# Optimization experiments

Hardware: AMD Instinct MI355X
Metric: run time of the kernel (lower is better)

The kernel has to match this reference:

```python
import jax, jax.numpy as jnp
import numpy as np

E = 8            # n_experts
TEMP = float(np.e)
N_ACTIVE = 5     # max(1, int(8 * 0.7))
EPS = 1e-8


def setup_inputs() -> dict:
    key = jax.random.key(0)
    ks = jax.random.split(key, 6)
    N, D, H, O = 8192, 1024, 2048, 1024

    def init(k, shape, fan_in):
        return (jax.random.normal(k, shape, jnp.float32) / np.sqrt(fan_in)).astype(jnp.float32)

    return {
        "x": jax.random.normal(ks[0], (N, D), jnp.float32),
        "gate_W": init(ks[1], (D, E), D),
        "gate_b": jnp.zeros((E,), jnp.float32),
        "W1": init(ks[2], (E, D, H), D),
        "b1": jnp.zeros((E, H), jnp.float32),
        "W2": init(ks[3], (E, H, H), H),
        "b2": jnp.zeros((E, H), jnp.float32),
        "W3": init(ks[4], (E, H, O), H),
        "b3": jnp.zeros((E, O), jnp.float32),
    }


def reference(x, gate_W, gate_b, W1, b1, W2, b2, W3, b3):
    # Boltzmann gate: softmax(scores / T), keep top n_active, renormalize.
    scores = (x @ gate_W + gate_b) / TEMP            # [N, E]
    probs = jax.nn.softmax(scores, axis=-1)          # [N, E]
    _, idx = jax.lax.top_k(probs, N_ACTIVE)          # [N, n_active]
    rows = jnp.arange(probs.shape[0])[:, None]
    mask = jnp.zeros_like(probs).at[rows, idx].set(1.0)
    w = probs * mask
    w = w / (w.sum(axis=-1, keepdims=True) + EPS)    # [N, E]

    # Dense all-expert MLP (dropout is identity in eval mode).
    h = jax.nn.relu(jnp.einsum('nd,edh->enh', x, W1) + b1[:, None, :])   # [E, N, H]
    h = jax.nn.relu(jnp.einsum('enh,ehk->enk', h, W2) + b2[:, None, :])  # [E, N, H]
    out = jnp.einsum('enh,eho->eno', h, W3) + b3[:, None, :]             # [E, N, O]

    # Weighted combine over experts.
    return jnp.einsum('ne,eno->no', w, out)          # [N, O]
```

## Files before the change

### kernel.cpp

```cpp
#include <hip/hip_runtime.h>

#define N_ROWS 8192
#define DIM_D  1024
#define DIM_H  2048
#define DIM_O  1024
#define NEXP   8
#define NACT   5
#define MAX_TILES 168

typedef _Float16 f16x8 __attribute__((ext_vector_type(8)));
typedef float    f32x4 __attribute__((ext_vector_type(4)));

__device__ __forceinline__ void gload_lds16(const void* g, void* l) {
  __builtin_amdgcn_global_load_lds(
      (const __attribute__((address_space(1))) void*)g,
      (__attribute__((address_space(3))) void*)l, 16, 0, 0);
}

__global__ void convert_x_kernel(const float* __restrict__ in,
                                 _Float16* __restrict__ out, int n) {
  int i = (blockIdx.x * 256 + threadIdx.x) * 8;
  if (i >= n) return;
  const float4 a = *(const float4*)(in + i);
  const float4 b = *(const float4*)(in + i + 4);
  f16x8 v;
  v[0] = (_Float16)a.x; v[1] = (_Float16)a.y; v[2] = (_Float16)a.z; v[3] = (_Float16)a.w;
  v[4] = (_Float16)b.x; v[5] = (_Float16)b.y; v[6] = (_Float16)b.z; v[7] = (_Float16)b.w;
  *(f16x8*)(out + i) = v;
}

__global__ void zero_f32_kernel(float* __restrict__ p, int n4) {
  int i = blockIdx.x * 256 + threadIdx.x;
  if (i < n4) ((float4*)p)[i] = make_float4(0.f, 0.f, 0.f, 0.f);
}
__global__ void zero_counts_kernel(int* __restrict__ cnt) {
  if (threadIdx.x < NEXP) cnt[threadIdx.x] = 0;
}

__global__ void transpose_to_f16(const float* __restrict__ in,
                                 _Float16* __restrict__ out, int R, int C) {
  in  += (size_t)blockIdx.z * R * C;
  out += (size_t)blockIdx.z * R * C;
  __shared__ float tile[32][33];
  const int tx = threadIdx.x & 31, ty = threadIdx.x >> 5;
  const int c0 = blockIdx.x * 32, r0 = blockIdx.y * 32;
#pragma unroll
  for (int j = 0; j < 32; j += 8)
    tile[ty + j][tx] = in[(size_t)(r0 + ty + j) * C + c0 + tx];
  __syncthreads();
#pragma unroll
  for (int j = 0; j < 32; j += 8)
    out[(size_t)(c0 + ty + j) * R + r0 + tx] = (_Float16)tile[tx][ty + j];
}

__global__ void gate_kernel(const float* __restrict__ x, const float* __restrict__ gW,
                            const float* __restrict__ gb, float* __restrict__ wout) {
  const int lane = threadIdx.x & 63;
  const int row  = blockIdx.x * 4 + (threadIdx.x >> 6);
  float acc[8] = {0.f,0.f,0.f,0.f,0.f,0.f,0.f,0.f};
  const float* xr = x + (size_t)row * DIM_D;
  for (int d = lane; d < DIM_D; d += 64) {
    float xv = xr[d];
    const float4* g4 = (const float4*)(gW + d * 8);
    float4 a = g4[0], b = g4[1];
    acc[0] += xv * a.x; acc[1] += xv * a.y; acc[2] += xv * a.z; acc[3] += xv * a.w;
    acc[4] += xv * b.x; acc[5] += xv * b.y; acc[6] += xv * b.z; acc[7] += xv * b.w;
  }
#pragma unroll
  for (int off = 32; off > 0; off >>= 1) {
#pragma unroll
    for (int e = 0; e < 8; ++e) acc[e] += __shfl_xor(acc[e], off);
  }
  const float invT = 0.36787944117144233f;
  float s[8], mx = -1e30f;
#pragma unroll
  for (int e = 0; e < 8; ++e) { s[e] = (acc[e] + gb[e]) * invT; mx = fmaxf(mx, s[e]); }
  float p[8], sum = 0.f;
#pragma unroll
  for (int e = 0; e < 8; ++e) { p[e] = expf(s[e] - mx); sum += p[e]; }
  float inv = 1.f / sum;
#pragma unroll
  for (int e = 0; e < 8; ++e) p[e] *= inv;
  unsigned keep = 0;
  for (int it = 0; it < NACT; ++it) {
    int best = 0; float bv = -1.f;
#pragma unroll
    for (int e = 0; e < 8; ++e)
      if (!(keep & (1u << e)) && p[e] > bv) { bv = p[e]; best = e; }
    keep |= 1u << best;
  }
  float ks = 0.f;
#pragma unroll
  for (int e = 0; e < 8; ++e) if (keep & (1u << e)) ks += p[e];
  const float winv = 1.f / (ks + 1e-8f);
  if (lane < 8)
    wout[(size_t)row * 8 + lane] = (keep & (1u << lane)) ? p[lane] * winv : 0.f;
}

__global__ void count_kernel(const float* __restrict__ wg, int* __restrict__ cnt) {
  const int row = blockIdx.x * 256 + threadIdx.x;
  const int lane = threadIdx.x & 63;
#pragma unroll
  for (int e = 0; e < NEXP; ++e) {
    const bool keep = wg[(size_t)row * 8 + e] > 0.f;
    unsigned long long m = __ballot(keep);
    if (lane == 0 && m) atomicAdd(&cnt[e], __popcll(m));
  }
}

__global__ void offsets_kernel(const int* __restrict__ cnt, int* __restrict__ cursor,
                               int* __restrict__ offs, int* __restrict__ ntiles,
                               int2* __restrict__ ttab, int* __restrict__ rlist) {
  __shared__ int soffs[NEXP], scnt[NEXP];
  if (threadIdx.x == 0) {
    int off = 0, k = 0;
    for (int e = 0; e < NEXP; ++e) {
      offs[e] = off; soffs[e] = off; scnt[e] = cnt[e];
      cursor[e] = 0;
      const int nt = (cnt[e] + 255) >> 8;
      for (int t2 = 0; t2 < nt; ++t2) { ttab[k] = make_int2(e, off + t2 * 256); ++k; }
      off += nt << 8;
    }
    *ntiles = k;
  }
  __syncthreads();
#pragma unroll
  for (int e = 0; e < NEXP; ++e) {
    const int lo = soffs[e] + scnt[e];
    const int hi = soffs[e] + ((scnt[e] + 255) & ~255);
    for (int i = lo + (int)threadIdx.x; i < hi; i += 256) rlist[i] = 0;
  }
}

__global__ void place_kernel(const float* __restrict__ wg, const int* __restrict__ offs,
                             int* __restrict__ cursor, int* __restrict__ rlist,
                             int* __restrict__ pos) {
  const int row = blockIdx.x * 256 + threadIdx.x;
  const int lane = threadIdx.x & 63;
#pragma unroll
  for (int e = 0; e < NEXP; ++e) {
    const bool keep = wg[(size_t)row * 8 + e] > 0.f;
    unsigned long long m = __ballot(keep);
    if (m) {
      const int leader = __ffsll(m) - 1;
      const int pre = __popcll(m & ((1ull << lane) - 1ull));
      int base = 0;
      if (lane == leader) base = atomicAdd(&cursor[e], __popcll(m));
      base = __shfl(base, leader);
      if (keep) {
        const int idx = offs[e] + base + pre;
        rlist[idx] = row;
        pos[(size_t)row * 8 + e] = idx;
      }
    }
  }
}

__global__ void combine_kernel(const float* __restrict__ wg, const int* __restrict__ pos,
                               const _Float16* __restrict__ y, float* __restrict__ out) {
  const int tid = blockIdx.x * 256 + threadIdx.x;
  const int row = tid >> 7, c8 = (tid & 127) * 8;
  float a[8] = {0.f,0.f,0.f,0.f,0.f,0.f,0.f,0.f};
#pragma unroll
  for (int e = 0; e < NEXP; ++e) {
    const float w = wg[(size_t)row * 8 + e];
    if (w > 0.f) {
      const int p = pos[(size_t)row * 8 + e];
      const f16x8 v = *(const f16x8*)(y + (size_t)p * DIM_O + c8);
#pragma unroll
      for (int j = 0; j < 8; ++j) a[j] += w * (float)v[j];
    }
  }
  float4* o4 = (float4*)(out + (size_t)row * DIM_O + c8);
  o4[0] = make_float4(a[0], a[1], a[2], a[3]);
  o4[1] = make_float4(a[4], a[5], a[6], a[7]);
}

#define MFMA16 __builtin_amdgcn_mfma_f32_16x16x32_f16
template <int MODE>
__global__ __launch_bounds__(512, 2) void gemm8(
    const _Float16* __restrict__ A, const _Float16* __restrict__ BtAll,
    _Float16* __restrict__ C, const float* __restrict__ biasAll,
    const int* __restrict__ rlist, const int2* __restrict__ ttab,
    const int* __restrict__ ntilesp, int N, int K) {
  const int ti = blockIdx.y;
  if (ti >= *ntilesp) return;
  const int2 tt = ttab[ti];
  const int e = tt.x, grow0 = tt.y;
  const int col0 = blockIdx.x * 256;

  __shared__ _Float16 sA[2][256 * 64];
  __shared__ _Float16 sB[2][256 * 64];

  const int t = threadIdx.x, wid = t >> 6, lane = t & 63;
  const int wm = wid >> 2, wn = wid & 3;
  const int l15 = lane & 15, lg = lane >> 4;

  const _Float16* Bt = BtAll + (size_t)e * N * K;

  const int srow = wid * 8 + (lane >> 3);
  const int scol = ((lane & 7) ^ (lane >> 3)) << 3;
  size_t arow[4], brow[4];
#pragma unroll
  for (int c = 0; c < 4; ++c) {
    const int r = c * 64 + srow;
    const int gr = (MODE == 0) ? rlist[grow0 + r] : (grow0 + r);
    arow[c] = (size_t)gr * K;
    brow[c] = (size_t)(col0 + r) * K;
  }
  const int ldst = wid * 512;

  auto STAGE = [&](int buf, int kt) {
    const int kofs = kt * 64 + scol;
#pragma unroll
    for (int c = 0; c < 4; ++c)
      gload_lds16(A + arow[c] + kofs, &sA[buf][c * 4096 + ldst]);
#pragma unroll
    for (int c = 0; c < 4; ++c)
      gload_lds16(Bt + brow[c] + kofs, &sB[buf][c * 4096 + ldst]);
  };

  const int ck0 = ((lg * 16) ^ ((l15 & 7) << 4)) >> 1;
  const int ck1 = ((64 + lg * 16) ^ ((l15 & 7) << 4)) >> 1;

  f32x4 acc[8][4] = {};
  const int NT = K >> 6;
  STAGE(0, 0);
  STAGE(1, 1);

  for (int tk = 0; tk < NT; ++tk) {
    const int buf = tk & 1;
    if (tk + 1 < NT) asm volatile("s_waitcnt vmcnt(8)" ::: "memory");
    else             asm volatile("s_waitcnt vmcnt(0)" ::: "memory");
    __builtin_amdgcn_sched_barrier(0);
    __builtin_amdgcn_s_barrier();
    __builtin_amdgcn_sched_barrier(0);

    const _Float16* pA = &sA[buf][wm * 128 * 64];
    const _Float16* pB = &sB[buf][wn * 64 * 64];

    f16x8 af[4][2], bf0[2][2], bf1[2][2];
#pragma unroll
    for (int m = 0; m < 4; ++m) {
      af[m][0] = *(const f16x8*)(pA + (m * 16 + l15) * 64 + ck0);
      af[m][1] = *(const f16x8*)(pA + (m * 16 + l15) * 64 + ck1);
    }
#pragma unroll
    for (int n = 0; n < 2; ++n) {
      bf0[n][0] = *(const f16x8*)(pB + (n * 16 + l15) * 64 + ck0);
      bf0[n][1] = *(const f16x8*)(pB + (n * 16 + l15) * 64 + ck1);
    }
    __builtin_amdgcn_s_setprio(1);
#pragma unroll
    for (int m = 0; m < 4; ++m)
#pragma unroll
      for (int n = 0; n < 2; ++n) {
        acc[m][n] = MFMA16(af[m][0], bf0[n][0], acc[m][n], 0, 0, 0);
        acc[m][n] = MFMA16(af[m][1], bf0[n][1], acc[m][n], 0, 0, 0);
      }
    __builtin_amdgcn_s_setprio(0);
#pragma unroll
    for (int n = 0; n < 2; ++n) {
      bf1[n][0] = *(const f16x8*)(pB + ((n + 2) * 16 + l15) * 64 + ck0);
      bf1[n][1] = *(const f16x8*)(pB + ((n + 2) * 16 + l15) * 64 + ck1);
    }
    __builtin_amdgcn_s_setprio(1);
#pragma unroll
    for (int m = 0; m < 4; ++m)
#pragma unroll
      for (int n = 0; n < 2; ++n) {
        acc[m][n + 2] = MFMA16(af[m][0], bf1[n][0], acc[m][n + 2], 0, 0, 0);
        acc[m][n + 2] = MFMA16(af[m][1], bf1[n][1], acc[m][n + 2], 0, 0, 0);
      }
    __builtin_amdgcn_s_setprio(0);
#pragma unroll
    for (int m = 0; m < 4; ++m) {
      af[m][0] = *(const f16x8*)(pA + ((m + 4) * 16 + l15) * 64 + ck0);
      af[m][1] = *(const f16x8*)(pA + ((m + 4) * 16 + l15) * 64 + ck1);
    }
    __builtin_amdgcn_s_setprio(1);
#pragma unroll
    for (int m = 0; m < 4; ++m)
#pragma unroll
      for (int n = 0; n < 2; ++n) {
        acc[m + 4][n] = MFMA16(af[m][0], bf0[n][0], acc[m + 4][n], 0, 0, 0);
        acc[m + 4][n] = MFMA16(af[m][1], bf0[n][1], acc[m + 4][n], 0, 0, 0);
      }
#pragma unroll
    for (int m = 0; m < 4; ++m)
#pragma unroll
      for (int n = 0; n < 2; ++n) {
        acc[m + 4][n + 2] = MFMA16(af[m][0], bf1[n][0], acc[m + 4][n + 2], 0, 0, 0);
        acc[m + 4][n + 2] = MFMA16(af[m][1], bf1[n][1], acc[m + 4][n + 2], 0, 0, 0);
      }
    __builtin_amdgcn_s_setprio(0);

    __builtin_amdgcn_sched_barrier(0);
    __builtin_amdgcn_s_barrier();
    __builtin_amdgcn_sched_barrier(0);
    if (tk + 2 < NT) STAGE(buf, tk + 2);
  }

  const float* bias = biasAll + (size_t)e * N;
  float bv[4];
#pragma unroll
  for (int n = 0; n < 4; ++n) bv[n] = bias[col0 + wn * 64 + n * 16 + l15];
#pragma unroll
  for (int mi = 0; mi < 8; ++mi) {
#pragma unroll
    for (int n = 0; n < 4; ++n) {
      const int gc = col0 + wn * 64 + n * 16 + l15;
#pragma unroll
      for (int r = 0; r < 4; ++r) {
        const int grow = grow0 + wm * 128 + mi * 16 + lg * 4 + r;
        const float v = acc[mi][n][r] + bv[n];
        C[(size_t)grow * N + gc] = (_Float16)((MODE == 2) ? v : fmaxf(v, 0.f));
      }
    }
  }
}

__global__ void compact_old(const float* __restrict__ wg, int* __restrict__ cnt,
                            int* __restrict__ rowlist) {
  const int row = blockIdx.x * 256 + threadIdx.x;
  const int lane = threadIdx.x & 63;
#pragma unroll
  for (int e = 0; e < NEXP; ++e) {
    const float w = wg[(size_t)row * 8 + e];
    const bool keep = (w > 0.f);
    unsigned long long m = __ballot(keep);
    if (m) {
      const int leader = __ffsll(m) - 1;
      const int pre = __popcll(m & ((1ull << lane) - 1ull));
      int base = 0;
      if (lane == leader) base = atomicAdd(&cnt[e], __popcll(m));
      base = __shfl(base, leader);
      if (keep) rowlist[e * N_ROWS + base + pre] = row;
    }
  }
}

template <int MODE>
__global__ __launch_bounds__(256, 2) void gemm_nt(
    const _Float16* __restrict__ A, const _Float16* __restrict__ Bt,
    void* __restrict__ Cout, const float* __restrict__ bias,
    const float* __restrict__ wg, const int* __restrict__ rlist,
    const int* __restrict__ cntp, int e, int N, int K) {
  const int M = *cntp;
  const int row0 = blockIdx.y * 128, col0 = blockIdx.x * 128;
  if (row0 >= M) return;
  __shared__ _Float16 sA[128 * 64];
  __shared__ _Float16 sB[128 * 64];
  const int t = threadIdx.x;
  const int w = t >> 6, lane = t & 63;
  const int wm = w >> 1, wn = w & 1;
  const int l15 = lane & 15, lg = lane >> 4;
  size_t arow[4];
#pragma unroll
  for (int i = 0; i < 4; ++i) {
    const int chunk = i * 256 + t;
    int li = row0 + (chunk >> 3);
    if (li >= M && MODE == 0) li = M - 1;
    const int gr = (MODE == 0) ? rlist[li] : li;
    arow[i] = (size_t)gr * K;
  }
  f32x4 acc[4][4] = {};
  for (int kt = 0; kt < K; kt += 64) {
    __syncthreads();
#pragma unroll
    for (int i = 0; i < 4; ++i) {
      const int chunk = i * 256 + t;
      const int cb = (chunk & 7) * 8;
      gload_lds16(A + arow[i] + kt + cb, sA + (i * 256 + w * 64) * 8);
    }
#pragma unroll
    for (int i = 0; i < 4; ++i) {
      const int chunk = i * 256 + t;
      const int r = chunk >> 3, cb = (chunk & 7) * 8;
      gload_lds16(Bt + (size_t)(col0 + r) * K + kt + cb, sB + (i * 256 + w * 64) * 8);
    }
    __syncthreads();
#pragma unroll
    for (int k2 = 0; k2 < 2; ++k2) {
      f16x8 af[4], bf[4];
#pragma unroll
      for (int m = 0; m < 4; ++m)
        af[m] = *(const f16x8*)(sA + (wm * 64 + m * 16 + l15) * 64 + k2 * 32 + lg * 8);
#pragma unroll
      for (int n = 0; n < 4; ++n)
        bf[n] = *(const f16x8*)(sB + (wn * 64 + n * 16 + l15) * 64 + k2 * 32 + lg * 8);
#pragma unroll
      for (int m = 0; m < 4; ++m)
#pragma unroll
        for (int n = 0; n < 4; ++n)
          acc[m][n] = MFMA16(af[m], bf[n], acc[m][n], 0, 0, 0);
    }
  }
#pragma unroll
  for (int m = 0; m < 4; ++m) {
#pragma unroll
    for (int n = 0; n < 4; ++n) {
      const int gc = col0 + wn * 64 + n * 16 + l15;
      const float bvv = bias[gc];
#pragma unroll
      for (int r = 0; r < 4; ++r) {
        const int gr = row0 + wm * 64 + m * 16 + lg * 4 + r;
        float v = acc[m][n][r] + bvv;
        if (MODE == 3) {
          if (gr < M) {
            const int orow = rlist[gr];
            atomicAdd((float*)Cout + (size_t)orow * N + gc,
                      wg[(size_t)orow * 8 + e] * v);
          }
        } else {
          ((_Float16*)Cout)[(size_t)gr * N + gc] = (_Float16)fmaxf(v, 0.f);
        }
      }
    }
  }
}

extern "C" void kernel_launch(void* const* d_in, const int* in_sizes, int n_in,
                              void* d_out, int out_size, void* d_ws, size_t ws_size,
                              hipStream_t stream) {
  const float* x  = (const float*)d_in[0];
  const float* gW = (const float*)d_in[1];
  const float* gb = (const float*)d_in[2];
  const float* W1 = (const float*)d_in[3];
  const float* b1 = (const float*)d_in[4];
  const float* W2 = (const float*)d_in[5];
  const float* b2 = (const float*)d_in[6];
  const float* W3 = (const float*)d_in[7];
  const float* b3 = (const float*)d_in[8];
  float* out = (float*)d_out;

  char* ws = (char*)d_ws;
  const bool big = (ws_size >= 0x1E100000ULL);

  if (big) {
    float* wgate   = (float*)ws;
    int*   meta    = (int*)(ws + 0x40000);
    int*   cnt     = meta;
    int*   cursor  = meta + 8;
    int*   offs    = meta + 16;
    int*   ntiles  = meta + 24;
    int2*  ttab    = (int2*)(meta + 32);
    int*   pos     = (int*)(ws + 0x80000);
    int*   rlistg  = (int*)(ws + 0xC0000);
    _Float16* xh   = (_Float16*)(ws + 0x100000);
    _Float16* h1   = (_Float16*)(ws + 0x1100000);
    _Float16* h2   = (_Float16*)(ws + 0xB900000);
    _Float16* wt1  = (_Float16*)(ws + 0x16100000);
    _Float16* wt2  = (_Float16*)(ws + 0x18100000);
    _Float16* wt3  = (_Float16*)(ws + 0x1C100000);
    _Float16* y    = h1;

    convert_x_kernel<<<(N_ROWS * DIM_D) / (256 * 8), 256, 0, stream>>>(x, xh, N_ROWS * DIM_D);
    gate_kernel<<<N_ROWS / 4, 256, 0, stream>>>(x, gW, gb, wgate);
    zero_counts_kernel<<<1, 64, 0, stream>>>(cnt);
    count_kernel<<<N_ROWS / 256, 256, 0, stream>>>(wgate, cnt);
    offsets_kernel<<<1, 256, 0, stream>>>(cnt, cursor, offs, ntiles, ttab, rlistg);
    place_kernel<<<N_ROWS / 256, 256, 0, stream>>>(wgate, offs, cursor, rlistg, pos);

    transpose_to_f16<<<dim3(DIM_H / 32, DIM_D / 32, NEXP), 256, 0, stream>>>(W1, wt1, DIM_D, DIM_H);
    transpose_to_f16<<<dim3(DIM_H / 32, DIM_H / 32, NEXP), 256, 0, stream>>>(W2, wt2, DIM_H, DIM_H);
    transpose_to_f16<<<dim3(DIM_O / 32, DIM_H / 32, NEXP), 256, 0, stream>>>(W3, wt3, DIM_H, DIM_O);

    gemm8<0><<<dim3(DIM_H / 256, MAX_TILES), 512, 0, stream>>>(
        xh, wt1, h1, b1, rlistg, ttab, ntiles, DIM_H, DIM_D);
    gemm8<1><<<dim3(DIM_H / 256, MAX_TILES), 512, 0, stream>>>(
        h1, wt2, h2, b2, rlistg, ttab, ntiles, DIM_H, DIM_H);
    gemm8<2><<<dim3(DIM_O / 256, MAX_TILES), 512, 0, stream>>>(
        h2, wt3, y, b3, rlistg, ttab, ntiles, DIM_O, DIM_H);

    combine_kernel<<<(N_ROWS * 128) / 256, 256, 0, stream>>>(wgate, pos, y, out);
  } else {
    float*    wgate = (float*)ws;
    int*      cnt   = (int*)(ws + 0x40000);
    int*      rlist = (int*)(ws + 0x80000);
    _Float16* xh    = (_Float16*)(ws + 0x100000);
    _Float16* h1    = (_Float16*)(ws + 0x1100000);
    _Float16* h2    = (_Float16*)(ws + 0x3100000);
    _Float16* wt1   = (_Float16*)(ws + 0x5100000);
    _Float16* wt2   = (_Float16*)(ws + 0x5500000);
    _Float16* wt3   = (_Float16*)(ws + 0x5D00000);

    convert_x_kernel<<<(N_ROWS * DIM_D) / (256 * 8), 256, 0, stream>>>(x, xh, N_ROWS * DIM_D);
    gate_kernel<<<N_ROWS / 4, 256, 0, stream>>>(x, gW, gb, wgate);
    zero_counts_kernel<<<1, 64, 0, stream>>>(cnt);
    compact_old<<<N_ROWS / 256, 256, 0, stream>>>(wgate, cnt, rlist);
    zero_f32_kernel<<<(N_ROWS * DIM_O / 4 + 255) / 256, 256, 0, stream>>>(out, N_ROWS * DIM_O / 4);

    for (int e = 0; e < NEXP; ++e) {
      transpose_to_f16<<<dim3(DIM_H / 32, DIM_D / 32), 256, 0, stream>>>(
          W1 + (size_t)e * DIM_D * DIM_H, wt1, DIM_D, DIM_H);
      transpose_to_f16<<<dim3(DIM_H / 32, DIM_H / 32), 256, 0, stream>>>(
          W2 + (size_t)e * DIM_H * DIM_H, wt2, DIM_H, DIM_H);
      transpose_to_f16<<<dim3(DIM_O / 32, DIM_H / 32), 256, 0, stream>>>(
          W3 + (size_t)e * DIM_H * DIM_O, wt3, DIM_H, DIM_O);
      const int* ce = cnt + e;
      const int* re = rlist + e * N_ROWS;
      gemm_nt<0><<<dim3(DIM_H / 128, N_ROWS / 128), 256, 0, stream>>>(
          xh, wt1, h1, b1 + (size_t)e * DIM_H, wgate, re, ce, e, DIM_H, DIM_D);
      gemm_nt<1><<<dim3(DIM_H / 128, N_ROWS / 128), 256, 0, stream>>>(
          h1, wt2, h2, b2 + (size_t)e * DIM_H, wgate, re, ce, e, DIM_H, DIM_H);
      gemm_nt<3><<<dim3(DIM_O / 128, N_ROWS / 128), 256, 0, stream>>>(
          h2, wt3, out, b3 + (size_t)e * DIM_O, wgate, re, ce, e, DIM_O, DIM_H);
    }
  }
}
```

Baseline: 1.081 ms.

## Interleave staged global-to-LDS loads between MFMA quarters and remap tiles per XCD

The GEMM main loop now splits each prefetch of the next-but-one K tile into pieces (A rows 0/2, all of B, A rows 1/3). These are issued between the four MFMA quarters, separated by extra barriers, once the corresponding LDS region has been read. This replaces a single bulk stage at the end of each iteration and is meant to overlap memory traffic with compute. Block IDs are also remapped so that consecutive blocks scheduled round-robin on the 8 XCDs work on the same row tile, which is meant to improve L2 reuse. In exchange there are more barriers per iteration, and the kernel always issues dummy loads of tile 0 in the tail iterations.

```diff
diff --git a/kernel.cpp b/kernel.cpp
--- a/kernel.cpp
+++ b/kernel.cpp
@@ -183,11 +183,15 @@
     _Float16* __restrict__ C, const float* __restrict__ biasAll,
     const int* __restrict__ rlist, const int2* __restrict__ ttab,
     const int* __restrict__ ntilesp, int N, int K) {
-  const int ti = blockIdx.y;
+  const int ncol = gridDim.x;
+  const int b = blockIdx.y * ncol + blockIdx.x;
+  const int xcd = b & 7, idx = b >> 3;
+  const int ti = xcd * (MAX_TILES / 8) + idx / ncol;
+  const int colt = idx % ncol;
   if (ti >= *ntilesp) return;
   const int2 tt = ttab[ti];
   const int e = tt.x, grow0 = tt.y;
-  const int col0 = blockIdx.x * 256;
+  const int col0 = colt * 256;
 
   __shared__ _Float16 sA[2][256 * 64];
   __shared__ _Float16 sB[2][256 * 64];
@@ -210,14 +214,16 @@
   }
   const int ldst = wid * 512;
 
-  auto STAGE = [&](int buf, int kt) {
+  auto STAGE_A2 = [&](int sbuf, int kt, int c0_, int c1_) {
     const int kofs = kt * 64 + scol;
+    gload_lds16(A + arow[c0_] + kofs, &sA[sbuf][c0_ * 4096 + ldst]);
+    gload_lds16(A + arow[c1_] + kofs, &sA[sbuf][c1_ * 4096 + ldst]);
+  };
+  auto STAGE_B4 = [&](int sbuf, int kt) {
+    const int kofs = kt * 64 + scol;
 #pragma unroll
     for (int c = 0; c < 4; ++c)
-      gload_lds16(A + arow[c] + kofs, &sA[buf][c * 4096 + ldst]);
-#pragma unroll
-    for (int c = 0; c < 4; ++c)
-      gload_lds16(Bt + brow[c] + kofs, &sB[buf][c * 4096 + ldst]);
+      gload_lds16(Bt + brow[c] + kofs, &sB[sbuf][c * 4096 + ldst]);
   };
 
   const int ck0 = ((lg * 16) ^ ((l15 & 7) << 4)) >> 1;
@@ -225,81 +231,102 @@
 
   f32x4 acc[8][4] = {};
   const int NT = K >> 6;
-  STAGE(0, 0);
-  STAGE(1, 1);
+  const int k1 = (NT > 1) ? 1 : 0;
+
+  STAGE_A2(0, 0, 0, 1); STAGE_A2(0, 0, 2, 3); STAGE_B4(0, 0);
+  STAGE_A2(1, k1, 0, 2); STAGE_B4(1, k1); STAGE_A2(1, k1, 1, 3);
 
   for (int tk = 0; tk < NT; ++tk) {
     const int buf = tk & 1;
-    if (tk + 1 < NT) asm volatile("s_waitcnt vmcnt(8)" ::: "memory");
-    else             asm volatile("s_waitcnt vmcnt(0)" ::: "memory");
-    __builtin_amdgcn_sched_barrier(0);
-    __builtin_amdgcn_s_barrier();
-    __builtin_amdgcn_sched_barrier(0);
-
+    const int s2 = (tk + 2 < NT) ? tk + 2 : 0;
     const _Float16* pA = &sA[buf][wm * 128 * 64];
     const _Float16* pB = &sB[buf][wn * 64 * 64];
-
-    f16x8 af[4][2], bf0[2][2], bf1[2][2];
+    f16x8 a0[4][2], a1[4][2], b0[2][2], b1[2][2];
+
+    asm volatile("s_waitcnt vmcnt(8)" ::: "memory");
+    __builtin_amdgcn_sched_barrier(0);
+    __builtin_amdgcn_s_barrier();
+    __builtin_amdgcn_sched_barrier(0);
 #pragma unroll
     for (int m = 0; m < 4; ++m) {
-      af[m][0] = *(const f16x8*)(pA + (m * 16 + l15) * 64 + ck0);
-      af[m][1] = *(const f16x8*)(pA + (m * 16 + l15) * 64 + ck1);
+      a0[m][0] = *(const f16x8*)(pA + (m * 16 + l15) * 64 + ck0);
+      a0[m][1] = *(const f16x8*)(pA + (m * 16 + l15) * 64 + ck1);
     }
 #pragma unroll
     for (int n = 0; n < 2; ++n) {
-      bf0[n][0] = *(const f16x8*)(pB + (n * 16 + l15) * 64 + ck0);
-      bf0[n][1] = *(const f16x8*)(pB + (n * 16 + l15) * 64 + ck1);
-    }
+      b0[n][0] = *(const f16x8*)(pB + (n * 16 + l15) * 64 + ck0);
+      b0[n][1] = *(const f16x8*)(pB + (n * 16 + l15) * 64 + ck1);
+    }
+    asm volatile("s_waitcnt lgkmcnt(0)" ::: "memory");
+    __builtin_amdgcn_sched_barrier(0);
     __builtin_amdgcn_s_setprio(1);
 #pragma unroll
     for (int m = 0; m < 4; ++m)
 #pragma unroll
       for (int n = 0; n < 2; ++n) {
-        acc[m][n] = MFMA16(af[m][0], bf0[n][0], acc[m][n], 0, 0, 0);
-        acc[m][n] = MFMA16(af[m][1], bf0[n][1], acc[m][n], 0, 0, 0);
+        acc[m][n] = MFMA16(a0[m][0], b0[n][0], acc[m][n], 0, 0, 0);
+        acc[m][n] = MFMA16(a0[m][1], b0[n][1], acc[m][n], 0, 0, 0);
       }
     __builtin_amdgcn_s_setprio(0);
+
+    __builtin_amdgcn_sched_barrier(0);
+    __builtin_amdgcn_s_barrier();
+    __builtin_amdgcn_sched_barrier(0);
 #pragma unroll
     for (int n = 0; n < 2; ++n) {
-      bf1[n][0] = *(const f16x8*)(pB + ((n + 2) * 16 + l15) * 64 + ck0);
-      bf1[n][1] = *(const f16x8*)(pB + ((n + 2) * 16 + l15) * 64 + ck1);
-    }
+      b1[n][0] = *(const f16x8*)(pB + ((n + 2) * 16 + l15) * 64 + ck0);
+      b1[n][1] = *(const f16x8*)(pB + ((n + 2) * 16 + l15) * 64 + ck1);
+    }
+    STAGE_A2(buf, s2, 0, 2);
+    asm volatile("s_waitcnt lgkmcnt(0)" ::: "memory");
+    __builtin_amdgcn_sched_barrier(0);
     __builtin_amdgcn_s_setprio(1);
 #pragma unroll
     for (int m = 0; m < 4; ++m)
 #pragma unroll
       for (int n = 0; n < 2; ++n) {
-        acc[m][n + 2] = MFMA16(af[m][0], bf1[n][0], acc[m][n + 2], 0, 0, 0);
-        acc[m][n + 2] = MFMA16(af[m][1], bf1[n][1], acc[m][n + 2], 0, 0, 0);
+        acc[m][n + 2] = MFMA16(a0[m][0], b1[n][0], acc[m][n + 2], 0, 0, 0);
+        acc[m][n + 2] = MFMA16(a0[m][1], b1[n][1], acc[m][n + 2], 0, 0, 0);
       }
     __builtin_amdgcn_s_setprio(0);
+
+    __builtin_amdgcn_sched_barrier(0);
+    __builtin_amdgcn_s_barrier();
+    __builtin_amdgcn_sched_barrier(0);
 #pragma unroll
     for (int m = 0; m < 4; ++m) {
-      af[m][0] = *(const f16x8*)(pA + ((m + 4) * 16 + l15) * 64 + ck0);
-      af[m][1] = *(const f16x8*)(pA + ((m + 4) * 16 + l15) * 64 + ck1);
-    }
+      a1[m][0] = *(const f16x8*)(pA + ((m + 4) * 16 + l15) * 64 + ck0);
+      a1[m][1] = *(const f16x8*)(pA + ((m + 4) * 16 + l15) * 64 + ck1);
+    }
+    STAGE_B4(buf, s2);
+    asm volatile("s_waitcnt lgkmcnt(0)" ::: "memory");
+    __builtin_amdgcn_sched_barrier(0);
     __builtin_amdgcn_s_setprio(1);
 #pragma unroll
     for (int m = 0; m < 4; ++m)
 #pragma unroll
       for (int n = 0; n < 2; ++n) {
-        acc[m + 4][n] = MFMA16(af[m][0], bf0[n][0], acc[m + 4][n], 0, 0, 0);
-        acc[m + 4][n] = MFMA16(af[m][1], bf0[n][1], acc[m + 4][n], 0, 0, 0);
-      }
+        acc[m + 4][n] = MFMA16(a1[m][0], b0[n][0], acc[m + 4][n], 0, 0, 0);
+        acc[m + 4][n] = MFMA16(a1[m][1], b0[n][1], acc[m + 4][n], 0, 0, 0);
+      }
+    __builtin_amdgcn_s_setprio(0);
+
+    __builtin_amdgcn_sched_barrier(0);
+    __builtin_amdgcn_s_barrier();
+    __builtin_amdgcn_sched_barrier(0);
+    STAGE_A2(buf, s2, 1, 3);
+    __builtin_amdgcn_s_setprio(1);
 #pragma unroll
     for (int m = 0; m < 4; ++m)
 #pragma unroll
       for (int n = 0; n < 2; ++n) {
-        acc[m + 4][n + 2] = MFMA16(af[m][0], bf1[n][0], acc[m + 4][n + 2], 0, 0, 0);
-        acc[m + 4][n + 2] = MFMA16(af[m][1], bf1[n][1], acc[m + 4][n + 2], 0, 0, 0);
+        acc[m + 4][n + 2] = MFMA16(a1[m][0], b1[n][0], acc[m + 4][n + 2], 0, 0, 0);
+        acc[m + 4][n + 2] = MFMA16(a1[m][1], b1[n][1], acc[m + 4][n + 2], 0, 0, 0);
       }
     __builtin_amdgcn_s_setprio(0);
-
-    __builtin_amdgcn_sched_barrier(0);
-    __builtin_amdgcn_s_barrier();
-    __builtin_amdgcn_sched_barrier(0);
-    if (tk + 2 < NT) STAGE(buf, tk + 2);
-  }
+  }
+
+  asm volatile("s_waitcnt vmcnt(0)" ::: "memory");
 
   const float* bias = biasAll + (size_t)e * N;
   float bv[4];
```

Result: slower. 1.108 ms (+2.5%).
